# Kernel optimization log

Measured on AMD Instinct MI355X. Metric: run time of the kernel, lower is better.

Reference implementation:

```python
import jax, jax.numpy as jnp
import numpy as np

N_ATOMS = 131072
N_MOLS = 4096
D = 128
N_DEPTH = 128
EPS = 1e-07
MEMBERSHIPS = np.array([(-1.645, 0.283), (-1.08, 0.17), (-0.739, 0.134), (-0.468, 0.118),
                        (-0.228, 0.114), (0.0, 0.114), (0.228, 0.114), (0.468, 0.118),
                        (0.739, 0.134), (1.08, 0.17), (1.645, 0.283)], dtype=np.float32)


def setup_inputs() -> dict:
    key = jax.random.key(0)
    k1, k2, k3, k4 = jax.random.split(key, 4)
    x = jax.random.normal(k1, (N_ATOMS, D), dtype=jnp.float32)
    atom_split = jnp.sort(jax.random.randint(k2, (N_ATOMS,), 0, N_MOLS)).astype(jnp.int64)
    W = jax.random.normal(k3, (D * 11, N_DEPTH), dtype=jnp.float32) * 0.02
    b = jax.random.normal(k4, (N_DEPTH,), dtype=jnp.float32) * 0.02
    return {"x": x, "atom_split": atom_split, "W": W, "b": b}


def reference(x, atom_split, W, b):
    means = jnp.asarray(MEMBERSHIPS[:, 0])          # [11]
    stds = jnp.asarray(MEMBERSHIPS[:, 1])           # [11]
    log_norm = jnp.log(stds * np.sqrt(2.0 * np.pi)) # [11]
    # Normal log_prob: -0.5*((x-m)/s)^2 - log(s*sqrt(2pi)); dist_max = log_prob(m) = -log_norm
    z = (x[:, :, None] - means) / stds              # [N, D, 11]
    logp = -0.5 * z * z - log_norm
    out = logp / (-log_norm)                        # divide by log_prob at mean
    out = (out + EPS) / (jnp.sum(out, axis=2, keepdims=True) + EPS)
    out = out.reshape(-1, D * 11)                   # [N, D*11]
    mols = jax.ops.segment_sum(out, atom_split, num_segments=N_MOLS)  # [M, D*11]
    return jnp.tanh(mols @ W + b)                   # [M, n_depth]
```

## Files before the change

### kernel.cpp

```cpp
#include <hip/hip_runtime.h>
#include <math.h>

#define N_ATOMS 131072
#define N_MOLS  4096
#define DFEAT   128
#define NK      11
#define KDIM3   384
#define N_DEPTH 128
#define EPS_F   1e-7f
#define MPB     8
#define TPB     512

__constant__ float c_means[NK] = {-1.645f, -1.08f, -0.739f, -0.468f, -0.228f,
                                  0.0f, 0.228f, 0.468f, 0.739f, 1.08f, 1.645f};
__constant__ float c_stds[NK]  = {0.283f, 0.17f, 0.134f, 0.118f, 0.114f,
                                  0.114f, 0.114f, 0.118f, 0.134f, 0.17f, 0.283f};


__global__ __launch_bounds__(256) void wxform_offsets_kernel(
    const float* __restrict__ W,
    const int*   __restrict__ split,
    float*       __restrict__ Bt,
    int*         __restrict__ offsets) {
  const int bid = blockIdx.x;
  const int tid = threadIdx.x;
  if (bid < 192) {
    int t = bid * 256 + tid;
    int n = t & 127;
    int row = t >> 7;
    int j = row >> 7;
    int d = row & 127;
    float acc = 0.0f;
#pragma unroll
    for (int k = 0; k < NK; ++k) {
      float m = c_means[k], s = c_stds[k];
      float a = 0.5f / (s * s * logf(s * 2.5066282746310002f));
      float coef = (j == 2) ? a
                 : (j == 1) ? (-2.0f * a * m)
                            : fmaf(a, m * m, 1.0f + EPS_F);
      acc = fmaf(coef, W[(size_t)(d * NK + k) * N_DEPTH + n], acc);
    }
    Bt[(size_t)row * N_DEPTH + n] = acc;
  } else {
    int t = (bid - 192) * 256 + tid;
    if (t <= N_MOLS) {
      int lo = 0, hi = N_ATOMS;
      while (lo < hi) { int mid = (lo + hi) >> 1; if (split[mid] < t) lo = mid + 1; else hi = mid; }
      offsets[t] = lo;
    }
  }
}

__global__ __launch_bounds__(TPB) void fused_sums_gemm_kernel(
    const float* __restrict__ x,
    const int*   __restrict__ offsets,
    const float* __restrict__ Bt,
    const float* __restrict__ bias,
    float*       __restrict__ out) {
  const int tid = threadIdx.x;
  const int m0  = blockIdx.x * MPB;

  __shared__ float As[MPB][KDIM3];
  __shared__ float comb[4][MPB][DFEAT];

  float C2 = 0.0f, C1 = 0.0f, C0 = 11.0f + EPS_F;
#pragma unroll
  for (int k = 0; k < NK; ++k) {
    float m_ = c_means[k], s_ = c_stds[k];
    float a = 0.5f / (s_ * s_ * logf(s_ * 2.5066282746310002f));
    C2 += a;
    C1 = fmaf(-2.0f * a, m_, C1);
    C0 = fmaf(a, m_ * m_, C0);
  }

  const int w    = tid >> 6;
  const int lane = tid & 63;
  const int fq   = lane & 31;
  const int h    = lane >> 5;

  const int start = offsets[m0 + w];
  const int end   = offsets[m0 + w + 1];

  float Sr[4]   = {0.f, 0.f, 0.f, 0.f};
  float Sxr[4]  = {0.f, 0.f, 0.f, 0.f};
  float Sxxr[4] = {0.f, 0.f, 0.f, 0.f};

  int a = start + h;
  for (; a + 2 < end; a += 4) {
    float4 v0 = *(const float4*)&x[(size_t)a * DFEAT + fq * 4];
    float4 v1 = *(const float4*)&x[(size_t)(a + 2) * DFEAT + fq * 4];
    float xv0[4] = {v0.x, v0.y, v0.z, v0.w};
    float xv1[4] = {v1.x, v1.y, v1.z, v1.w};
#pragma unroll
    for (int q = 0; q < 4; ++q) {
      float den0 = fmaf(fmaf(C2, xv0[q], C1), xv0[q], C0);
      float den1 = fmaf(fmaf(C2, xv1[q], C1), xv1[q], C0);
      float r0 = __builtin_amdgcn_rcpf(den0);
      float r1 = __builtin_amdgcn_rcpf(den1);
      float u0 = xv0[q] * r0;
      float u1 = xv1[q] * r1;
      Sr[q]  += r0 + r1;
      Sxr[q] += u0 + u1;
      Sxxr[q] = fmaf(xv0[q], u0, Sxxr[q]);
      Sxxr[q] = fmaf(xv1[q], u1, Sxxr[q]);
    }
  }
  for (; a < end; a += 2) {
    float4 v = *(const float4*)&x[(size_t)a * DFEAT + fq * 4];
    float xv[4] = {v.x, v.y, v.z, v.w};
#pragma unroll
    for (int q = 0; q < 4; ++q) {
      float den = fmaf(fmaf(C2, xv[q], C1), xv[q], C0);
      float r   = __builtin_amdgcn_rcpf(den);
      float u   = xv[q] * r;
      Sr[q]  += r;
      Sxr[q] += u;
      Sxxr[q] = fmaf(xv[q], u, Sxxr[q]);
    }
  }

#pragma unroll
  for (int q = 0; q < 4; ++q) {
    Sr[q]   += __shfl_xor(Sr[q],   32, 64);
    Sxr[q]  += __shfl_xor(Sxr[q],  32, 64);
    Sxxr[q] += __shfl_xor(Sxxr[q], 32, 64);
  }

  if (h == 0) {
    *(float4*)&As[w][fq * 4]             = make_float4(Sr[0],  Sr[1],  Sr[2],  Sr[3]);
    *(float4*)&As[w][DFEAT + fq * 4]     = make_float4(Sxr[0], Sxr[1], Sxr[2], Sxr[3]);
    *(float4*)&As[w][2 * DFEAT + fq * 4] = make_float4(Sxxr[0],Sxxr[1],Sxxr[2],Sxxr[3]);
  }
  __syncthreads();

  const int n  = tid & 127;
  const int hh = tid >> 7;
  const int kbase = hh * (KDIM3 / 4);

  float pacc[MPB];
#pragma unroll
  for (int i = 0; i < MPB; ++i) pacc[i] = 0.0f;

#pragma unroll 2
  for (int kk = 0; kk < KDIM3 / 4; kk += 4) {
    int k = kbase + kk;
    float b0 = Bt[(size_t)(k + 0) * N_DEPTH + n];
    float b1 = Bt[(size_t)(k + 1) * N_DEPTH + n];
    float b2 = Bt[(size_t)(k + 2) * N_DEPTH + n];
    float b3 = Bt[(size_t)(k + 3) * N_DEPTH + n];
#pragma unroll
    for (int i = 0; i < MPB; ++i) {
      float4 av = *(const float4*)&As[i][k];
      pacc[i] = fmaf(av.x, b0, pacc[i]);
      pacc[i] = fmaf(av.y, b1, pacc[i]);
      pacc[i] = fmaf(av.z, b2, pacc[i]);
      pacc[i] = fmaf(av.w, b3, pacc[i]);
    }
  }

#pragma unroll
  for (int i = 0; i < MPB; ++i) comb[hh][i][n] = pacc[i];
  __syncthreads();

#pragma unroll
  for (int off = 0; off < (MPB * DFEAT) / TPB; ++off) {
    int idx = off * TPB + tid;
    int i  = idx >> 7;
    int nn = idx & 127;
    float v = comb[0][i][nn] + comb[1][i][nn] + comb[2][i][nn] + comb[3][i][nn]
            + bias[nn];
    out[(size_t)(m0 + i) * N_DEPTH + nn] = tanhf(v);
  }
}

extern "C" void kernel_launch(void* const* d_in, const int* in_sizes, int n_in,
                              void* d_out, int out_size, void* d_ws, size_t ws_size,
                              hipStream_t stream) {
  const float* x     = (const float*)d_in[0];
  const int*   split = (const int*)d_in[1];
  const float* W     = (const float*)d_in[2];
  const float* bias  = (const float*)d_in[3];
  float* out = (float*)d_out;

  float* Bt      = (float*)d_ws;
  int*   offsets = (int*)((char*)d_ws + (size_t)KDIM3 * N_DEPTH * 4);

  wxform_offsets_kernel<<<dim3(192 + 17), dim3(256), 0, stream>>>(W, split, Bt, offsets);
  fused_sums_gemm_kernel<<<dim3(N_MOLS / MPB), dim3(TPB), 0, stream>>>(x, offsets, Bt, bias, out);
}
```

Baseline: 113.4 us.

## Unroll atom loop to four loads, scatter offsets from split boundaries, add occupancy hint

The atom accumulation loop now issues four independent float4 loads per iteration instead of two, giving more memory-level parallelism in the bandwidth-bound x reduction. Segment offsets are now written by one thread per atom at each boundary change, replacing per-molecule binary searches. This needs 512 extra blocks in the setup kernel. A launch_bounds occupancy hint of 8 is added, which may constrain register allocation.

```diff
diff --git a/kernel.cpp b/kernel.cpp
--- a/kernel.cpp
+++ b/kernel.cpp
@@ -10,6 +10,7 @@
 #define EPS_F   1e-7f
 #define MPB     8
 #define TPB     512
+#define SCAN_BLOCKS (N_ATOMS / 256)
 
 __constant__ float c_means[NK] = {-1.645f, -1.08f, -0.739f, -0.468f, -0.228f,
                                   0.0f, 0.228f, 0.468f, 0.739f, 1.08f, 1.645f};
@@ -42,16 +43,16 @@
     }
     Bt[(size_t)row * N_DEPTH + n] = acc;
   } else {
-    int t = (bid - 192) * 256 + tid;
-    if (t <= N_MOLS) {
-      int lo = 0, hi = N_ATOMS;
-      while (lo < hi) { int mid = (lo + hi) >> 1; if (split[mid] < t) lo = mid + 1; else hi = mid; }
-      offsets[t] = lo;
-    }
+    int a = (bid - 192) * 256 + tid;
+    int cur  = split[a];
+    int prev = (a == 0) ? -1 : split[a - 1];
+    for (int j = prev + 1; j <= cur; ++j) offsets[j] = a;
+    if (a == N_ATOMS - 1)
+      for (int j = cur + 1; j <= N_MOLS; ++j) offsets[j] = N_ATOMS;
   }
 }
 
-__global__ __launch_bounds__(TPB) void fused_sums_gemm_kernel(
+__global__ __launch_bounds__(TPB, 8) void fused_sums_gemm_kernel(
     const float* __restrict__ x,
     const int*   __restrict__ offsets,
     const float* __restrict__ Bt,
@@ -85,28 +86,9 @@
   float Sxr[4]  = {0.f, 0.f, 0.f, 0.f};
   float Sxxr[4] = {0.f, 0.f, 0.f, 0.f};
 
-  int a = start + h;
-  for (; a + 2 < end; a += 4) {
-    float4 v0 = *(const float4*)&x[(size_t)a * DFEAT + fq * 4];
-    float4 v1 = *(const float4*)&x[(size_t)(a + 2) * DFEAT + fq * 4];
-    float xv0[4] = {v0.x, v0.y, v0.z, v0.w};
-    float xv1[4] = {v1.x, v1.y, v1.z, v1.w};
-#pragma unroll
-    for (int q = 0; q < 4; ++q) {
-      float den0 = fmaf(fmaf(C2, xv0[q], C1), xv0[q], C0);
-      float den1 = fmaf(fmaf(C2, xv1[q], C1), xv1[q], C0);
-      float r0 = __builtin_amdgcn_rcpf(den0);
-      float r1 = __builtin_amdgcn_rcpf(den1);
-      float u0 = xv0[q] * r0;
-      float u1 = xv1[q] * r1;
-      Sr[q]  += r0 + r1;
-      Sxr[q] += u0 + u1;
-      Sxxr[q] = fmaf(xv0[q], u0, Sxxr[q]);
-      Sxxr[q] = fmaf(xv1[q], u1, Sxxr[q]);
-    }
-  }
-  for (; a < end; a += 2) {
-    float4 v = *(const float4*)&x[(size_t)a * DFEAT + fq * 4];
+  const float* xp = x + fq * 4;
+
+  auto proc = [&](float4 v) {
     float xv[4] = {v.x, v.y, v.z, v.w};
 #pragma unroll
     for (int q = 0; q < 4; ++q) {
@@ -117,6 +99,19 @@
       Sxr[q] += u;
       Sxxr[q] = fmaf(xv[q], u, Sxxr[q]);
     }
+  };
+
+  int a = start + h;
+  for (; a + 6 < end; a += 8) {
+    float4 v0 = *(const float4*)&xp[(size_t)(a + 0) * DFEAT];
+    float4 v1 = *(const float4*)&xp[(size_t)(a + 2) * DFEAT];
+    float4 v2 = *(const float4*)&xp[(size_t)(a + 4) * DFEAT];
+    float4 v3 = *(const float4*)&xp[(size_t)(a + 6) * DFEAT];
+    proc(v0); proc(v1); proc(v2); proc(v3);
+  }
+  for (; a < end; a += 2) {
+    float4 v = *(const float4*)&xp[(size_t)a * DFEAT];
+    proc(v);
   }
 
 #pragma unroll
@@ -185,6 +180,6 @@
   float* Bt      = (float*)d_ws;
   int*   offsets = (int*)((char*)d_ws + (size_t)KDIM3 * N_DEPTH * 4);
 
-  wxform_offsets_kernel<<<dim3(192 + 17), dim3(256), 0, stream>>>(W, split, Bt, offsets);
+  wxform_offsets_kernel<<<dim3(192 + SCAN_BLOCKS), dim3(256), 0, stream>>>(W, split, Bt, offsets);
   fused_sums_gemm_kernel<<<dim3(N_MOLS / MPB), dim3(TPB), 0, stream>>>(x, offsets, Bt, bias, out);
 }
```

After: 112.7 us. Within noise of the previous version (-0.6%).
